# Kernel tuning notes

Hardware: AMD Instinct MI355X
Metric: run time of the kernel (lower is better)

The kernel has to match this reference:

```python
import jax, jax.numpy as jnp
import numpy as np

N_NODES = 100000
N_EDGES = 3200000
F = 32          # n_node_features
L = 50          # n_node_labels
EL = 10         # n_edge_labels
K = 16          # out_dim (graph_data.num_classes)


def setup_inputs() -> dict:
    key = jax.random.key(0)
    ks = jax.random.split(key, 12)
    x = jax.random.normal(ks[0], (N_NODES, F), dtype=jnp.float32)
    node_labels = jax.random.randint(ks[1], (N_NODES,), 0, L, dtype=jnp.int32)
    edge_src = jax.random.randint(ks[2], (N_EDGES,), 0, N_NODES, dtype=jnp.int32)
    edge_dst = jax.random.randint(ks[3], (N_EDGES,), 0, N_NODES, dtype=jnp.int32)
    edge_labels = jax.random.randint(ks[4], (N_EDGES,), 0, EL, dtype=jnp.int32)
    s = 0.1
    W1 = jax.random.normal(ks[5], (L, L, EL), dtype=jnp.float32) * s
    b1 = jax.random.normal(ks[6], (L,), dtype=jnp.float32) * s
    W2 = jax.random.normal(ks[7], (L, L, EL), dtype=jnp.float32) * s
    b2 = jax.random.normal(ks[8], (L,), dtype=jnp.float32) * s
    W3 = jax.random.normal(ks[9], (L, L, EL), dtype=jnp.float32) * s
    b3 = jax.random.normal(ks[10], (L,), dtype=jnp.float32) * s
    kr1, kr2 = jax.random.split(ks[11])
    Wr = jax.random.normal(kr1, (L, F, K), dtype=jnp.float32) * s
    br = jax.random.normal(kr2, (K,), dtype=jnp.float32) * s
    return {"x": x, "W1": W1, "b1": b1, "W2": W2, "b2": b2, "W3": W3, "b3": b3,
            "Wr": Wr, "br": br, "node_labels": node_labels,
            "edge_src": edge_src, "edge_dst": edge_dst, "edge_labels": edge_labels}


def _conv(x, W, b, node_labels, edge_src, edge_dst, edge_labels):
    # weight_rule_wf: per-edge scalar weight indexed by (src label, dst label, edge label)
    w_e = W[node_labels[edge_src], node_labels[edge_dst], edge_labels]  # [E]
    msgs = w_e[:, None] * x[edge_src]                                   # [E, F]
    agg = jax.ops.segment_sum(msgs, edge_dst, num_segments=x.shape[0])  # [N, F]
    # node_label_rule bias: per-node bias indexed by node label, then Tanh
    return jnp.tanh(agg + b[node_labels][:, None])


def reference(x, W1, b1, W2, b2, W3, b3, Wr, br,
              node_labels, edge_src, edge_dst, edge_labels):
    h = _conv(x, W1, b1, node_labels, edge_src, edge_dst, edge_labels)
    h = _conv(h, W2, b2, node_labels, edge_src, edge_dst, edge_labels)
    h = _conv(h, W3, b3, node_labels, edge_src, edge_dst, edge_labels)
    # GraphResizeLayer (node_label_rule): out[k] = sum_i Wr[label_i, f, k] * h[i, f] + br[k]
    # equivalent efficient form: pre-aggregate node features by label, then contract.
    sums = jax.ops.segment_sum(h, node_labels, num_segments=Wr.shape[0])  # [L, F]
    out = jnp.tanh(jnp.einsum('lf,lfk->k', sums, Wr) + br)                # [K]
    return out
```

## Files before the change

### kernel.cpp

```cpp
#include <hip/hip_runtime.h>
#include <hip/hip_bf16.h>
#include <hip/hip_fp8.h>

#define NN 100000
#define NE 3200000
#define FF 32
#define LL 50
#define ELB 10
#define KK 16

#define CH 8192
#define NBLK_P1 391
#define NBUK 391
#define CAP 9216

typedef float floatx2 __attribute__((ext_vector_type(2)));

__device__ __forceinline__ float fast_tanh(float x) {
    float e = __expf(2.0f * x);
    return 1.0f - 2.0f / (e + 1.0f);
}

__global__ __launch_bounds__(512) void p1_scatter(const int* __restrict__ esrc,
                                                  const int* __restrict__ edst,
                                                  const int* __restrict__ elab,
                                                  const float* __restrict__ x,
                                                  unsigned* __restrict__ xb,
                                                  int* __restrict__ cursor,
                                                  unsigned* __restrict__ recs) {
    __shared__ int lcnt[NBUK];
    __shared__ int lofs[NBUK];
    __shared__ int lbase[NBUK];
    __shared__ int sc[512];
    __shared__ unsigned srec[CH];
    __shared__ unsigned sgad[CH];
    int tid = threadIdx.x;
    for (int i = blockIdx.x * 512 + tid; i < NN * FF / 4; i += NBLK_P1 * 512) {
        float4 v = ((const float4*)x)[i];
        __hip_fp8_e4m3 a(v.x), b(v.y), c(v.z), d(v.w);
        xb[i] = (unsigned)a.__x | ((unsigned)b.__x << 8) |
                ((unsigned)c.__x << 16) | ((unsigned)d.__x << 24);
    }
    for (int i = tid; i < NBUK; i += 512) lcnt[i] = 0;
    __syncthreads();
    long e0 = (long)blockIdx.x * CH;
    long rem = NE - e0;
    int cnt = rem < CH ? (int)rem : CH;
    int nq = cnt >> 2;
    const int4* edst4 = (const int4*)(edst + e0);
    const int4* esrc4 = (const int4*)(esrc + e0);
    const int4* elab4 = (const int4*)(elab + e0);
    for (int i = tid; i < nq; i += 512) {
        int4 d = edst4[i];
        atomicAdd(&lcnt[d.x >> 8], 1);
        atomicAdd(&lcnt[d.y >> 8], 1);
        atomicAdd(&lcnt[d.z >> 8], 1);
        atomicAdd(&lcnt[d.w >> 8], 1);
    }
    __syncthreads();
    sc[tid] = (tid < NBUK) ? lcnt[tid] : 0;
    __syncthreads();
    for (int ofs = 1; ofs < 512; ofs <<= 1) {
        int t = (tid >= ofs) ? sc[tid - ofs] : 0;
        __syncthreads();
        sc[tid] += t;
        __syncthreads();
    }
    if (tid < NBUK) {
        int c = lcnt[tid];
        lofs[tid] = sc[tid] - c;
        lbase[tid] = c ? atomicAdd(&cursor[tid], c) : 0;
        lcnt[tid] = 0;
    }
    __syncthreads();
    for (int i = tid; i < nq; i += 512) {
        int4 s4 = esrc4[i];
        int4 l4 = elab4[i];
        int4 d4 = edst4[i];
#pragma unroll
        for (int k = 0; k < 4; ++k) {
            int s  = (&s4.x)[k];
            int d  = (&d4.x)[k];
            int el = (&l4.x)[k];
            int b = d >> 8;
            int pos = atomicAdd(&lcnt[b], 1);
            int slot = lofs[b] + pos;
            srec[slot] = ((unsigned)s << 12) | ((unsigned)el << 8) | (unsigned)(d & 255);
            int rel = lbase[b] + pos;
            sgad[slot] = (rel < CAP) ? (unsigned)(b * CAP + rel) : 0xFFFFFFFFu;
        }
    }
    __syncthreads();
    for (int i = tid; i < cnt; i += 512) {
        unsigned g = sgad[i];
        if (g != 0xFFFFFFFFu)
            recs[g] = srec[i];
    }
}

__global__ __launch_bounds__(512) void p2_local(const int* __restrict__ cursor,
                                                const unsigned* __restrict__ recs,
                                                const int* __restrict__ labels,
                                                unsigned* __restrict__ packed,
                                                int* __restrict__ gstart,
                                                int* __restrict__ gcnt) {
    __shared__ int deg[256], loff[256], lcur[256], sc[256], labd[256];
    int b = blockIdx.x, tid = threadIdx.x;
    int base = b * CAP;
    int n = cursor[b];
    if (n > CAP) n = CAP;
    if (tid < 256) {
        int node = (b << 8) + tid;
        deg[tid] = 0;
        lcur[tid] = 0;
        labd[tid] = (node < NN) ? labels[node] : 0;
    }
    __syncthreads();
    for (int i = tid; i < n; i += 512)
        atomicAdd(&deg[(int)(recs[base + i] & 255)], 1);
    __syncthreads();
    if (tid < 256) sc[tid] = deg[tid];
    __syncthreads();
    for (int ofs = 1; ofs < 256; ofs <<= 1) {
        int t = (tid >= ofs && tid < 256) ? sc[tid - ofs] : 0;
        __syncthreads();
        if (tid < 256) sc[tid] += t;
        __syncthreads();
    }
    if (tid < 256) {
        loff[tid] = sc[tid] - deg[tid];
        int node = (b << 8) + tid;
        if (node < NN) { gstart[node] = base + loff[tid]; gcnt[node] = deg[tid]; }
    }
    __syncthreads();
    for (int i = tid; i < n; i += 512) {
        unsigned r = recs[base + i];
        int dl  = (int)(r & 255);
        int el  = (int)((r >> 8) & 15);
        int src = (int)(r >> 12);
        int widx = labels[src] * (LL * ELB) + labd[dl] * ELB + el;
        int ofs = atomicAdd(&lcur[dl], 1);
        packed[base + loff[dl] + ofs] = ((unsigned)widx << 17) | (unsigned)src;
    }
}

__global__ __launch_bounds__(256) void conv_kernel(const unsigned char* __restrict__ xin,
                                                   unsigned char* __restrict__ hout,
                                                   const int* __restrict__ gstart,
                                                   const int* __restrict__ gcnt,
                                                   const unsigned* __restrict__ packed,
                                                   const float* __restrict__ Wtab,
                                                   const float* __restrict__ bias,
                                                   const int* __restrict__ labels) {
    __shared__ unsigned stage[8][64];
    int tid = threadIdx.x;
    int hw = tid >> 5, lane = tid & 31;
    int node = (blockIdx.x << 3) + hw;
    int s = gstart[node];
    int n = gcnt[node];
    int eg = lane >> 3;
    int fg = (lane & 7) << 2;
    float4 acc = {0.f, 0.f, 0.f, 0.f};
    for (int base = 0; base < n; base += 32) {
        float w = 0.f;
        unsigned so = 0u;
        int idx = base + lane;
        if (idx < n) {
            unsigned p = packed[s + idx];
            w = Wtab[p >> 17];
            so = (p & 0x1FFFFu) << 5;
        }
        ((uint2*)&stage[hw][0])[lane] = make_uint2(__float_as_uint(w), so);
        __builtin_amdgcn_wave_barrier();
#pragma unroll
        for (int j = 0; j < 8; ++j) {
            uint2 ws = ((const uint2*)&stage[hw][0])[j * 4 + eg];
            unsigned pv = *(const unsigned*)(xin + ws.y + fg);
            floatx2 lo = __builtin_amdgcn_cvt_pk_f32_fp8((int)pv, false);
            floatx2 hi = __builtin_amdgcn_cvt_pk_f32_fp8((int)pv, true);
            float we = __uint_as_float(ws.x);
            acc.x += we * lo.x;
            acc.y += we * lo.y;
            acc.z += we * hi.x;
            acc.w += we * hi.y;
        }
        __builtin_amdgcn_wave_barrier();
    }
    acc.x += __shfl_xor(acc.x, 8);  acc.y += __shfl_xor(acc.y, 8);
    acc.z += __shfl_xor(acc.z, 8);  acc.w += __shfl_xor(acc.w, 8);
    acc.x += __shfl_xor(acc.x, 16); acc.y += __shfl_xor(acc.y, 16);
    acc.z += __shfl_xor(acc.z, 16); acc.w += __shfl_xor(acc.w, 16);
    if (lane < 8) {
        float bb = bias[labels[node]];
        __hip_fp8_e4m3 q0(fast_tanh(acc.x + bb));
        __hip_fp8_e4m3 q1(fast_tanh(acc.y + bb));
        __hip_fp8_e4m3 q2(fast_tanh(acc.z + bb));
        __hip_fp8_e4m3 q3(fast_tanh(acc.w + bb));
        unsigned pk = (unsigned)q0.__x | ((unsigned)q1.__x << 8) |
                      ((unsigned)q2.__x << 16) | ((unsigned)q3.__x << 24);
        ((unsigned*)(hout + ((long)node << 5)))[lane] = pk;
    }
}

__global__ __launch_bounds__(256) void lsum_kernel(const unsigned* __restrict__ h,
                                                   const int* __restrict__ labels,
                                                   float* __restrict__ sums) {
    __shared__ float ls[LL * FF];
    int tid = threadIdx.x;
    for (int i = tid; i < LL * FF; i += 256) ls[i] = 0.f;
    __syncthreads();
    for (int i = blockIdx.x * 256 + tid; i < NN * 8; i += gridDim.x * 256) {
        unsigned pv = h[i];
        int nodei = i >> 3;
        int fb = (i & 7) << 2;
        int l = labels[nodei];
        floatx2 lo = __builtin_amdgcn_cvt_pk_f32_fp8((int)pv, false);
        floatx2 hi = __builtin_amdgcn_cvt_pk_f32_fp8((int)pv, true);
        float* bp = &ls[l * FF + fb];
        atomicAdd(bp + 0, lo.x);
        atomicAdd(bp + 1, lo.y);
        atomicAdd(bp + 2, hi.x);
        atomicAdd(bp + 3, hi.y);
    }
    __syncthreads();
    for (int i = tid; i < LL * FF; i += 256) atomicAdd(&sums[i], ls[i]);
}

__global__ __launch_bounds__(256) void resize_kernel(const float* __restrict__ sums,
                                                     const float* __restrict__ Wr,
                                                     const float* __restrict__ br,
                                                     float* __restrict__ out) {
    __shared__ float red[256][KK];
    int tid = threadIdx.x;
    float acc[KK];
#pragma unroll
    for (int k = 0; k < KK; ++k) acc[k] = 0.f;
    for (int p = tid; p < LL * FF; p += 256) {
        float sv = sums[p];
#pragma unroll
        for (int k = 0; k < KK; ++k) acc[k] += sv * Wr[p * KK + k];
    }
#pragma unroll
    for (int k = 0; k < KK; ++k) red[tid][k] = acc[k];
    __syncthreads();
    for (int sft = 128; sft > 0; sft >>= 1) {
        if (tid < sft) {
#pragma unroll
            for (int k = 0; k < KK; ++k) red[tid][k] += red[tid + sft][k];
        }
        __syncthreads();
    }
    if (tid < KK) out[tid] = fast_tanh(red[0][tid] + br[tid]);
}

extern "C" void kernel_launch(void* const* d_in, const int* in_sizes, int n_in,
                              void* d_out, int out_size, void* d_ws, size_t ws_size,
                              hipStream_t stream) {
    const float* x   = (const float*)d_in[0];
    const float* W1  = (const float*)d_in[1];
    const float* b1  = (const float*)d_in[2];
    const float* W2  = (const float*)d_in[3];
    const float* b2  = (const float*)d_in[4];
    const float* W3  = (const float*)d_in[5];
    const float* b3  = (const float*)d_in[6];
    const float* Wr  = (const float*)d_in[7];
    const float* br  = (const float*)d_in[8];
    const int* labels = (const int*)d_in[9];
    const int* esrc   = (const int*)d_in[10];
    const int* edst   = (const int*)d_in[11];
    const int* elab   = (const int*)d_in[12];
    float* out = (float*)d_out;

    char* ws = (char*)d_ws;
    size_t o = 0;
    auto alloc = [&](size_t bytes) -> void* {
        void* p = ws + o;
        o += (bytes + 255) & ~(size_t)255;
        return p;
    };
    char* regionA = (char*)alloc((size_t)NBUK * CAP * sizeof(unsigned));
    unsigned* recs = (unsigned*)regionA;
    unsigned char* h1 = (unsigned char*)regionA;
    unsigned char* h2 = (unsigned char*)(regionA + (size_t)NN * FF);

    unsigned* packed = (unsigned*)alloc((size_t)NBUK * CAP * sizeof(unsigned));
    unsigned* xb     = (unsigned*)alloc((size_t)NN * FF);
    int* cursor = (int*)alloc(NBUK * sizeof(int));
    float* sums = (float*)alloc(LL * FF * sizeof(float));
    int* gstart = (int*)alloc(NN * sizeof(int));
    int* gcnt   = (int*)alloc(NN * sizeof(int));

    size_t msz = (size_t)((char*)sums - (char*)cursor) + LL * FF * sizeof(float);
    hipMemsetAsync(cursor, 0, msz, stream);

    p1_scatter<<<NBLK_P1, 512, 0, stream>>>(esrc, edst, elab, x, xb, cursor, recs);
    p2_local<<<NBUK, 512, 0, stream>>>(cursor, recs, labels, packed, gstart, gcnt);

    conv_kernel<<<NN / 8, 256, 0, stream>>>((const unsigned char*)xb, h1, gstart, gcnt, packed, W1, b1, labels);
    conv_kernel<<<NN / 8, 256, 0, stream>>>(h1, h2, gstart, gcnt, packed, W2, b2, labels);
    conv_kernel<<<NN / 8, 256, 0, stream>>>(h2, h1, gstart, gcnt, packed, W3, b3, labels);

    lsum_kernel<<<256, 256, 0, stream>>>((const unsigned*)h1, labels, sums);
    resize_kernel<<<1, 256, 0, stream>>>(sums, Wr, br, out);
}
```

Measured before the change: 292.2 us.

## Precompute per-edge fp16 weights for all three layers into 64-bit edge records

The three weight tables are interleaved into a float4 table during the scatter pass. The local-sort pass then resolves each edge's weight index once and packs fp16 weights for layers 1–3 plus the 17-bit source id into a 64-bit record. Each conv layer selects its weight by mode, which removes the dependent Wtab gather from the inner edge loop. In exchange, each conv reads 8-byte instead of 4-byte edge records, the sort pass gains an extra gather, and weights are rounded to fp16, with layer 3 losing one more mantissa bit.

```diff
diff --git a/kernel.cpp b/kernel.cpp
--- a/kernel.cpp
+++ b/kernel.cpp
@@ -1,5 +1,6 @@
 #include <hip/hip_runtime.h>
 #include <hip/hip_bf16.h>
+#include <hip/hip_fp16.h>
 #include <hip/hip_fp8.h>
 
 #define NN 100000
@@ -8,6 +9,7 @@
 #define LL 50
 #define ELB 10
 #define KK 16
+#define NWIDX (LL * LL * ELB)
 
 #define CH 8192
 #define NBLK_P1 391
@@ -25,6 +27,10 @@
                                                   const int* __restrict__ edst,
                                                   const int* __restrict__ elab,
                                                   const float* __restrict__ x,
+                                                  const float* __restrict__ W1,
+                                                  const float* __restrict__ W2,
+                                                  const float* __restrict__ W3,
+                                                  float4* __restrict__ Wi,
                                                   unsigned* __restrict__ xb,
                                                   int* __restrict__ cursor,
                                                   unsigned* __restrict__ recs) {
@@ -41,6 +47,8 @@
         xb[i] = (unsigned)a.__x | ((unsigned)b.__x << 8) |
                 ((unsigned)c.__x << 16) | ((unsigned)d.__x << 24);
     }
+    for (int i = blockIdx.x * 512 + tid; i < NWIDX; i += NBLK_P1 * 512)
+        Wi[i] = make_float4(W1[i], W2[i], W3[i], 0.f);
     for (int i = tid; i < NBUK; i += 512) lcnt[i] = 0;
     __syncthreads();
     long e0 = (long)blockIdx.x * CH;
@@ -101,7 +109,8 @@
 __global__ __launch_bounds__(512) void p2_local(const int* __restrict__ cursor,
                                                 const unsigned* __restrict__ recs,
                                                 const int* __restrict__ labels,
-                                                unsigned* __restrict__ packed,
+                                                const float4* __restrict__ Wi,
+                                                unsigned long long* __restrict__ ed,
                                                 int* __restrict__ gstart,
                                                 int* __restrict__ gcnt) {
     __shared__ int deg[256], loff[256], lcur[256], sc[256], labd[256];
@@ -139,8 +148,14 @@
         int el  = (int)((r >> 8) & 15);
         int src = (int)(r >> 12);
         int widx = labels[src] * (LL * ELB) + labd[dl] * ELB + el;
+        float4 wv = Wi[widx];
+        unsigned long long h1 = __half_as_ushort(__float2half(wv.x));
+        unsigned long long h2 = __half_as_ushort(__float2half(wv.y));
+        unsigned long long h3 = __half_as_ushort(__float2half(wv.z)) >> 1;
+        unsigned long long e = h1 | (h2 << 16) | (h3 << 32)
+                             | ((unsigned long long)(unsigned)src << 47);
         int ofs = atomicAdd(&lcur[dl], 1);
-        packed[base + loff[dl] + ofs] = ((unsigned)widx << 17) | (unsigned)src;
+        ed[base + loff[dl] + ofs] = e;
     }
 }
 
@@ -148,10 +163,10 @@
                                                    unsigned char* __restrict__ hout,
                                                    const int* __restrict__ gstart,
                                                    const int* __restrict__ gcnt,
-                                                   const unsigned* __restrict__ packed,
-                                                   const float* __restrict__ Wtab,
+                                                   const unsigned long long* __restrict__ ed,
                                                    const float* __restrict__ bias,
-                                                   const int* __restrict__ labels) {
+                                                   const int* __restrict__ labels,
+                                                   const int wmode) {
     __shared__ unsigned stage[8][64];
     int tid = threadIdx.x;
     int hw = tid >> 5, lane = tid & 31;
@@ -166,9 +181,13 @@
         unsigned so = 0u;
         int idx = base + lane;
         if (idx < n) {
-            unsigned p = packed[s + idx];
-            w = Wtab[p >> 17];
-            so = (p & 0x1FFFFu) << 5;
+            unsigned long long e = ed[s + idx];
+            unsigned short h;
+            if (wmode == 0)      h = (unsigned short)e;
+            else if (wmode == 1) h = (unsigned short)(e >> 16);
+            else                 h = (unsigned short)(((e >> 32) & 0x7FFFull) << 1);
+            w = __half2float(__ushort_as_half(h));
+            so = (unsigned)(e >> 47) << 5;
         }
         ((uint2*)&stage[hw][0])[lane] = make_uint2(__float_as_uint(w), so);
         __builtin_amdgcn_wave_barrier();
@@ -283,8 +302,9 @@
     unsigned char* h1 = (unsigned char*)regionA;
     unsigned char* h2 = (unsigned char*)(regionA + (size_t)NN * FF);
 
-    unsigned* packed = (unsigned*)alloc((size_t)NBUK * CAP * sizeof(unsigned));
-    unsigned* xb     = (unsigned*)alloc((size_t)NN * FF);
+    unsigned long long* ed = (unsigned long long*)alloc((size_t)NBUK * CAP * sizeof(unsigned long long));
+    unsigned* xb = (unsigned*)alloc((size_t)NN * FF);
+    float4* Wi   = (float4*)alloc((size_t)NWIDX * sizeof(float4));
     int* cursor = (int*)alloc(NBUK * sizeof(int));
     float* sums = (float*)alloc(LL * FF * sizeof(float));
     int* gstart = (int*)alloc(NN * sizeof(int));
@@ -293,12 +313,12 @@
     size_t msz = (size_t)((char*)sums - (char*)cursor) + LL * FF * sizeof(float);
     hipMemsetAsync(cursor, 0, msz, stream);
 
-    p1_scatter<<<NBLK_P1, 512, 0, stream>>>(esrc, edst, elab, x, xb, cursor, recs);
-    p2_local<<<NBUK, 512, 0, stream>>>(cursor, recs, labels, packed, gstart, gcnt);
-
-    conv_kernel<<<NN / 8, 256, 0, stream>>>((const unsigned char*)xb, h1, gstart, gcnt, packed, W1, b1, labels);
-    conv_kernel<<<NN / 8, 256, 0, stream>>>(h1, h2, gstart, gcnt, packed, W2, b2, labels);
-    conv_kernel<<<NN / 8, 256, 0, stream>>>(h2, h1, gstart, gcnt, packed, W3, b3, labels);
+    p1_scatter<<<NBLK_P1, 512, 0, stream>>>(esrc, edst, elab, x, W1, W2, W3, Wi, xb, cursor, recs);
+    p2_local<<<NBUK, 512, 0, stream>>>(cursor, recs, labels, Wi, ed, gstart, gcnt);
+
+    conv_kernel<<<NN / 8, 256, 0, stream>>>((const unsigned char*)xb, h1, gstart, gcnt, ed, b1, labels, 0);
+    conv_kernel<<<NN / 8, 256, 0, stream>>>(h1, h2, gstart, gcnt, ed, b2, labels, 1);
+    conv_kernel<<<NN / 8, 256, 0, stream>>>(h2, h1, gstart, gcnt, ed, b3, labels, 2);
 
     lsum_kernel<<<256, 256, 0, stream>>>((const unsigned*)h1, labels, sums);
     resize_kernel<<<1, 256, 0, stream>>>(sums, Wr, br, out);
```

After: 296.0 us. No clear change (+1.3%).
